# Optimization experiments

Hardware: AMD Instinct MI355X
Metric: run time of the kernel (lower is better)

## Reference

```python
import jax, jax.numpy as jnp
import numpy as np

SIM_THRESHOLD = 0.5   # similarity_threshold
LAMBDA = 0.1          # lambda_weight default


def setup_inputs() -> dict:
    key = jax.random.key(0)
    ks = jax.random.split(key, 8)
    B, T, C, P = 8, 1024, 1024, 100
    return {
        "attention_scores": jax.random.normal(ks[0], (B, T, T), jnp.float32),
        "context": jax.random.normal(ks[1], (B, C), jnp.float32),
        "triggers": jax.random.normal(ks[2], (P, C), jnp.float32),
        "biases": jax.random.uniform(ks[3], (P, T, T), jnp.float32),
        "confidences": jnp.ones((P,), jnp.float32),
        "W1": jax.random.normal(ks[4], (2 * C, C), jnp.float32) * (1.0 / np.sqrt(2 * C)),
        "b1": jnp.zeros((C,), jnp.float32),
        "W2": jax.random.normal(ks[5], (C,), jnp.float32) * (1.0 / np.sqrt(C)),
        "b2": jnp.zeros((1,), jnp.float32),
    }


def reference(attention_scores, context, triggers, biases, confidences, W1, b1, W2, b2):
    C = context.shape[-1]
    # combined = cat([context, trigger]) @ W1 == context @ W1[:C] + trigger @ W1[C:]
    ctx_h = context @ W1[:C]              # (B, C)
    trg_h = triggers @ W1[C:]             # (P, C)
    h = jax.nn.relu(ctx_h[:, None, :] + trg_h[None, :, :] + b1)   # (B, P, C)
    logits = h @ W2 + b2[0]               # (B, P)
    scores = jax.nn.sigmoid(logits).mean(axis=0)                  # (P,) mean over batch
    # match: only patterns with score > threshold contribute, weighted by score*confidence
    weights = jnp.where(scores > SIM_THRESHOLD, scores * confidences, 0.0)  # (P,)
    reasoning_bias = jnp.einsum("p,pij->ij", weights, biases)     # (T, T)
    return attention_scores + LAMBDA * reasoning_bias[None, :, :]
```

## Files before the change

### kernel.cpp

```cpp
#include <hip/hip_runtime.h>
#include <hip/hip_bf16.h>
#include <math.h>

#define BD 8
#define TD 1024
#define CD 1024
#define PD 100
#define KS 16
#define KW (CD / KS)
#define SEG 2048
#define TT (TD * TD)
#define SPLITQ 48
#define LAMBDA 0.1f
#define SIM_THR 0.5f

typedef float f4 __attribute__((ext_vector_type(4)));

__device__ float g_pctx[KS][BD][CD];
__device__ float g_ptrg[KS][PD][CD];
__device__ float g_ctxb[BD][CD];
__device__ float g_wd[PD];

__global__ __launch_bounds__(256) void hidden_kernel(const float* __restrict__ context,
                                                     const float* __restrict__ triggers,
                                                     const float* __restrict__ W1) {
    const int c  = blockIdx.x * 256 + threadIdx.x;
    const int kz = blockIdx.z;
    const int k0 = kz * KW;
    const bool is_ctx = (blockIdx.y == 0);
    const int  ych = blockIdx.y - 1;
    const float* __restrict__ W1p = is_ctx ? W1 : (W1 + (size_t)CD * CD);
    const float* __restrict__ src = is_ctx ? context : (triggers + (size_t)ych * 10 * CD);
    float* __restrict__ dst = is_ctx ? &g_pctx[kz][0][0] : &g_ptrg[kz][ych * 10][0];
    const int nrows = is_ctx ? 8 : 10;

    __shared__ float s_src[10][KW];
    for (int t = threadIdx.x; t < 10 * KW; t += 256) {
        const int r = t >> 6, k = t & (KW - 1);
        s_src[r][k] = src[(size_t)(r < nrows ? r : 0) * CD + k0 + k];
    }
    __syncthreads();

    float acc[10];
#pragma unroll
    for (int i = 0; i < 10; ++i) acc[i] = 0.f;

#pragma unroll 8
    for (int kk = 0; kk < KW; ++kk) {
        const float wv = W1p[(size_t)(k0 + kk) * CD + c];
#pragma unroll
        for (int i = 0; i < 10; ++i)
            acc[i] = fmaf(s_src[i][kk], wv, acc[i]);
    }
#pragma unroll
    for (int i = 0; i < 10; ++i)
        if (i < nrows) dst[(size_t)i * CD + c] = acc[i];
}

__global__ __launch_bounds__(256) void ctxsum_kernel(const float* __restrict__ b1) {
    const int idx = blockIdx.x * 256 + threadIdx.x;
    const int b = idx >> 10, c = idx & (CD - 1);
    float v = b1[c];
#pragma unroll
    for (int kz = 0; kz < KS; ++kz) v += g_pctx[kz][b][c];
    g_ctxb[b][c] = v;
}

__global__ __launch_bounds__(512) void score_kernel(const float* __restrict__ W2,
                                                    const float* __restrict__ b2,
                                                    const float* __restrict__ conf) {
    const int p = blockIdx.x;
    __shared__ float s_h[CD];
    __shared__ float s_logit[BD];

    for (int c = threadIdx.x; c < CD; c += 512) {
        float v = 0.f;
#pragma unroll
        for (int kz = 0; kz < KS; ++kz) v += g_ptrg[kz][p][c];
        s_h[c] = v;
    }
    __syncthreads();

    const int b = threadIdx.x >> 6, lane = threadIdx.x & 63;
    float sum = 0.f;
    for (int c = lane; c < CD; c += 64) {
        const float v = s_h[c] + g_ctxb[b][c];
        sum = fmaf(fmaxf(v, 0.f), W2[c], sum);
    }
#pragma unroll
    for (int off = 32; off > 0; off >>= 1) sum += __shfl_down(sum, off);
    if (lane == 0) s_logit[b] = sum + b2[0];
    __syncthreads();
    if (threadIdx.x == 0) {
        float s = 0.f;
#pragma unroll
        for (int bb = 0; bb < BD; ++bb) s += 1.f / (1.f + expf(-s_logit[bb]));
        s *= (1.f / BD);
        g_wd[p] = (s > SIM_THR) ? s * conf[p] * LAMBDA : 0.f;
    }
}

__global__ __launch_bounds__(256) void out_kernel(const float* __restrict__ attn,
                                                  const float* __restrict__ biases,
                                                  float* __restrict__ out) {
    __shared__ float    s_w[PD];
    __shared__ unsigned s_off[PD];
    __shared__ int      s_n;
    __shared__ float    s_part[4][SEG];

    if (threadIdx.x < 64) {
        const int lane = threadIdx.x;
        const float w0 = g_wd[lane];
        const float w1 = (lane < PD - 64) ? g_wd[lane + 64] : 0.f;
        const unsigned long long m0 = __ballot(w0 != 0.f);
        const unsigned long long m1 = __ballot(w1 != 0.f);
        const unsigned long long below = (1ull << lane) - 1;
        const int c0 = __popcll(m0);
        if (w0 != 0.f) {
            const int i = __popcll(m0 & below);
            s_w[i] = w0; s_off[i] = (unsigned)(lane * TT);
        }
        if (w1 != 0.f) {
            const int i = c0 + __popcll(m1 & below);
            s_w[i] = w1; s_off[i] = (unsigned)((lane + 64) * TT);
        }
        if (lane == 0) s_n = c0 + __popcll(m1);
    }
    __syncthreads();
    const int n = s_n;

    const int wv = threadIdx.x >> 6, lane = threadIdx.x & 63;
    const size_t seg = (size_t)blockIdx.x * SEG;

    f4 acc[8];
#pragma unroll
    for (int j = 0; j < 8; ++j) acc[j] = (f4){0.f, 0.f, 0.f, 0.f};

    for (int t = wv; t < n; t += 4) {
        const float w = s_w[t];
        const float* bp = biases + (size_t)s_off[t] + seg + (size_t)lane * 4;
        f4 v[8];
        if (s_off[t] < (unsigned)(SPLITQ * TT)) {
#pragma unroll
            for (int j = 0; j < 8; ++j) v[j] = *(const f4*)(bp + j * 256);
        } else {
#pragma unroll
            for (int j = 0; j < 8; ++j)
                v[j] = __builtin_nontemporal_load((const f4*)(bp + j * 256));
        }
#pragma unroll
        for (int j = 0; j < 8; ++j) {
            acc[j].x = fmaf(w, v[j].x, acc[j].x);
            acc[j].y = fmaf(w, v[j].y, acc[j].y);
            acc[j].z = fmaf(w, v[j].z, acc[j].z);
            acc[j].w = fmaf(w, v[j].w, acc[j].w);
        }
    }

#pragma unroll
    for (int j = 0; j < 8; ++j)
        *(f4*)&s_part[wv][j * 256 + lane * 4] = acc[j];
    __syncthreads();

    const int e = threadIdx.x * 8;
    f4 r0 = (f4){0.f, 0.f, 0.f, 0.f}, r1 = r0;
#pragma unroll
    for (int w2 = 0; w2 < 4; ++w2) {
        r0 += *(const f4*)&s_part[w2][e];
        r1 += *(const f4*)&s_part[w2][e + 4];
    }

#pragma unroll
    for (int b = 0; b < BD; ++b) {
        const size_t off = (size_t)b * TT + seg + (size_t)e;
        const f4 a0 = *(const f4*)(attn + off);
        const f4 a1 = *(const f4*)(attn + off + 4);
        __builtin_nontemporal_store(a0 + r0, (f4*)(out + off));
        __builtin_nontemporal_store(a1 + r1, (f4*)(out + off + 4));
    }
}

extern "C" void kernel_launch(void* const* d_in, const int* in_sizes, int n_in,
                              void* d_out, int out_size, void* d_ws, size_t ws_size,
                              hipStream_t stream) {
    const float* attn     = (const float*)d_in[0];
    const float* context  = (const float*)d_in[1];
    const float* triggers = (const float*)d_in[2];
    const float* biases   = (const float*)d_in[3];
    const float* conf     = (const float*)d_in[4];
    const float* W1       = (const float*)d_in[5];
    const float* b1       = (const float*)d_in[6];
    const float* W2       = (const float*)d_in[7];
    const float* b2       = (const float*)d_in[8];
    float* out = (float*)d_out;

    hipLaunchKernelGGL(hidden_kernel, dim3(CD / 256, 11, KS), dim3(256), 0, stream,
                       context, triggers, W1);
    hipLaunchKernelGGL(ctxsum_kernel, dim3(BD * CD / 256), dim3(256), 0, stream, b1);
    hipLaunchKernelGGL(score_kernel, dim3(PD), dim3(512), 0, stream, W2, b2, conf);
    hipLaunchKernelGGL(out_kernel, dim3(TT / SEG), dim3(256), 0, stream, attn, biases, out);
}
```

Baseline: 103.0 us.

## Fuse split-K reduction into hidden kernel via last-block atomic counter

Replaces the separate ctxsum kernel and the in-score-kernel trigger reduction with a last-block-done pattern. Each hidden_kernel block bumps a per-tile atomic counter, and the block that finishes last sums the 16 K-split partials for context and triggers. This removes one kernel launch and the redundant reduction work in score_kernel. It adds thread fences and atomics, and the counter relies on modulo-16 wraparound across calls, which is never reset.

```diff
diff --git a/kernel.cpp b/kernel.cpp
--- a/kernel.cpp
+++ b/kernel.cpp
@@ -16,14 +16,17 @@
 
 typedef float f4 __attribute__((ext_vector_type(4)));
 
-__device__ float g_pctx[KS][BD][CD];
-__device__ float g_ptrg[KS][PD][CD];
-__device__ float g_ctxb[BD][CD];
-__device__ float g_wd[PD];
+__device__ float    g_pctx[KS][BD][CD];
+__device__ float    g_ptrg[KS][PD][CD];
+__device__ float    g_ctxb[BD][CD];
+__device__ float    g_trgh[PD][CD];
+__device__ float    g_wd[PD];
+__device__ unsigned g_cnt[44];
 
 __global__ __launch_bounds__(256) void hidden_kernel(const float* __restrict__ context,
                                                      const float* __restrict__ triggers,
-                                                     const float* __restrict__ W1) {
+                                                     const float* __restrict__ W1,
+                                                     const float* __restrict__ b1) {
     const int c  = blockIdx.x * 256 + threadIdx.x;
     const int kz = blockIdx.z;
     const int k0 = kz * KW;
@@ -35,6 +38,7 @@
     const int nrows = is_ctx ? 8 : 10;
 
     __shared__ float s_src[10][KW];
+    __shared__ bool  s_last;
     for (int t = threadIdx.x; t < 10 * KW; t += 256) {
         const int r = t >> 6, k = t & (KW - 1);
         s_src[r][k] = src[(size_t)(r < nrows ? r : 0) * CD + k0 + k];
@@ -55,36 +59,45 @@
 #pragma unroll
     for (int i = 0; i < 10; ++i)
         if (i < nrows) dst[(size_t)i * CD + c] = acc[i];
-}
-
-__global__ __launch_bounds__(256) void ctxsum_kernel(const float* __restrict__ b1) {
-    const int idx = blockIdx.x * 256 + threadIdx.x;
-    const int b = idx >> 10, c = idx & (CD - 1);
-    float v = b1[c];
-#pragma unroll
-    for (int kz = 0; kz < KS; ++kz) v += g_pctx[kz][b][c];
-    g_ctxb[b][c] = v;
+
+    __syncthreads();
+    if (threadIdx.x == 0) {
+        __threadfence();
+        const unsigned old = atomicAdd(&g_cnt[blockIdx.y * 4 + blockIdx.x], 1u);
+        s_last = ((old & 15u) == 15u);
+    }
+    __syncthreads();
+    if (s_last) {
+        __threadfence();
+        if (is_ctx) {
+            for (int r = 0; r < BD; ++r) {
+                float v = b1[c];
+#pragma unroll
+                for (int kz2 = 0; kz2 < KS; ++kz2) v += g_pctx[kz2][r][c];
+                g_ctxb[r][c] = v;
+            }
+        } else {
+            for (int r = 0; r < 10; ++r) {
+                const int p = ych * 10 + r;
+                float v = 0.f;
+#pragma unroll
+                for (int kz2 = 0; kz2 < KS; ++kz2) v += g_ptrg[kz2][p][c];
+                g_trgh[p][c] = v;
+            }
+        }
+    }
 }
 
 __global__ __launch_bounds__(512) void score_kernel(const float* __restrict__ W2,
                                                     const float* __restrict__ b2,
                                                     const float* __restrict__ conf) {
     const int p = blockIdx.x;
-    __shared__ float s_h[CD];
     __shared__ float s_logit[BD];
-
-    for (int c = threadIdx.x; c < CD; c += 512) {
-        float v = 0.f;
-#pragma unroll
-        for (int kz = 0; kz < KS; ++kz) v += g_ptrg[kz][p][c];
-        s_h[c] = v;
-    }
-    __syncthreads();
 
     const int b = threadIdx.x >> 6, lane = threadIdx.x & 63;
     float sum = 0.f;
     for (int c = lane; c < CD; c += 64) {
-        const float v = s_h[c] + g_ctxb[b][c];
+        const float v = g_trgh[p][c] + g_ctxb[b][c];
         sum = fmaf(fmaxf(v, 0.f), W2[c], sum);
     }
 #pragma unroll
@@ -194,9 +207,8 @@
     const float* b2       = (const float*)d_in[8];
     float* out = (float*)d_out;
 
-    hipLaunchKernelGGL(hidden_kernel, dim3(CD / 256, 11, KS), dim3(256), 0, stream,
-                       context, triggers, W1);
-    hipLaunchKernelGGL(ctxsum_kernel, dim3(BD * CD / 256), dim3(256), 0, stream, b1);
+    hipLaunchKernelGGL(hidden_kernel, dim3(4, 11, KS), dim3(256), 0, stream,
+                       context, triggers, W1, b1);
     hipLaunchKernelGGL(score_kernel, dim3(PD), dim3(512), 0, stream, W2, b2, conf);
     hipLaunchKernelGGL(out_kernel, dim3(TT / SEG), dim3(256), 0, stream, attn, biases, out);
 }
```

Measured after the change: 131.1 us. 1.27x slower.
